# Performance work log

Hardware: AMD Instinct MI355X
Metric: run time of the kernel (lower is better)

## Reference

```python
import jax, jax.numpy as jnp
import numpy as np

CHANNELS = 64
HIDDEN = 1024
LAYERS = 24
NODE_TYPES = 19
BN_EPS = 1e-5

N_NODES = 200000
N_EDGES = 800000
N_RULES = 50000


def setup_inputs() -> dict:
    key = jax.random.key(0)
    ks = jax.random.split(key, 16)
    nodes = jax.random.randint(ks[0], (N_NODES,), 0, NODE_TYPES)
    sources = jax.random.randint(ks[1], (N_EDGES,), 0, N_NODES)
    targets = jax.random.randint(ks[2], (N_EDGES,), 0, N_NODES)
    rules = jax.random.randint(ks[3], (N_RULES,), 0, N_NODES)
    f32 = jnp.float32
    emb = jax.random.normal(ks[4], (NODE_TYPES, CHANNELS), f32)
    # per-layer, per-direction (out/back) Conv params, stacked [LAYERS, 2, ...]
    W = jax.random.normal(ks[5], (LAYERS, 2, CHANNELS, CHANNELS), f32) * 0.125  # ~xavier
    b = jax.random.normal(ks[6], (LAYERS, 2, CHANNELS), f32) * 0.01
    gamma = 1.0 + 0.1 * jax.random.normal(ks[7], (LAYERS, 2, CHANNELS), f32)
    beta = 0.01 * jax.random.normal(ks[8], (LAYERS, 2, CHANNELS), f32)
    rmean = 0.01 * jax.random.normal(ks[9], (LAYERS, 2, CHANNELS), f32)
    rvar = jax.random.uniform(ks[10], (LAYERS, 2, CHANNELS), f32, 0.5, 1.5)
    Wh = jax.random.normal(ks[11], (HIDDEN, CHANNELS), f32) * 0.05
    bh = jax.random.normal(ks[12], (HIDDEN,), f32) * 0.01
    Wo = jax.random.normal(ks[13], (1, HIDDEN), f32) * 0.03
    return {"nodes": nodes, "sources": sources, "targets": targets, "rules": rules,
            "emb": emb, "W": W, "b": b, "gamma": gamma, "beta": beta,
            "rmean": rmean, "rvar": rvar, "Wh": Wh, "bh": bh, "Wo": Wo}


def reference(nodes, sources, targets, rules, emb, W, b, gamma, beta, rmean, rvar, Wh, bh, Wo):
    n = nodes.shape[0]

    def conv(x, src, tgt, Wi, bi, g, be, rm, rv):
        # scatter_mean of gathered source features onto target nodes
        s = jax.ops.segment_sum(x[src], tgt, num_segments=n)            # [n, C]
        cnt = jax.ops.segment_sum(jnp.ones(src.shape, x.dtype), tgt, num_segments=n)
        m = s / jnp.maximum(cnt, 1.0)[:, None]
        # eval-mode BatchNorm1d (running stats) fused as affine
        xn = (m - rm) * (g * jax.lax.rsqrt(rv + BN_EPS)) + be
        return jax.nn.relu(xn @ Wi.T + bi)

    def layer(x, p):
        Wl, bl, gl, bel, rml, rvl = p
        out = conv(x, sources, targets, Wl[0], bl[0], gl[0], bel[0], rml[0], rvl[0])
        back = conv(x, targets, sources, Wl[1], bl[1], gl[1], bel[1], rml[1], rvl[1])
        return x + out + back, None

    x = emb[nodes]                                                      # [n, C]
    x, _ = jax.lax.scan(layer, x, (W, b, gamma, beta, rmean, rvar))
    h = jax.nn.relu(x[rules] @ Wh.T + bh)                               # [R, HIDDEN]
    return (h @ Wo.T)[:, 0]                                             # [R]
```

## Files before the change

kernel.cpp:

```cpp
#include <hip/hip_runtime.h>

#define N_NODES 200000
#define N_EDGES 800000
#define N_RULES 50000
#define NLAYERS 24
#define SCAN_NB 196
#define RP_STRIDE 200064

typedef short bf16x8 __attribute__((ext_vector_type(8)));
typedef float floatx4 __attribute__((ext_vector_type(4)));

__device__ __forceinline__ unsigned short f2bf(float f) {
  unsigned int b = __float_as_uint(f);
  b += 0x7FFFu + ((b >> 16) & 1u);
  return (unsigned short)(b >> 16);
}
__device__ __forceinline__ float bf2f(unsigned short u) {
  return __uint_as_float(((unsigned int)u) << 16);
}


__global__ void k_hist(const int* __restrict__ src, const int* __restrict__ tgt,
                       int* __restrict__ deg_out, int* __restrict__ deg_back) {
  int e = blockIdx.x * 256 + threadIdx.x;
  atomicAdd(&deg_out[tgt[e]], 1);
  atomicAdd(&deg_back[src[e]], 1);
}

__global__ void k_scanA(const int* __restrict__ deg, int* __restrict__ part) {
  int y = blockIdx.y;
  const int* d = deg + y * N_NODES;
  __shared__ int sh[256];
  int t = threadIdx.x;
  int base = blockIdx.x * 1024 + t * 4;
  int s = 0;
  #pragma unroll
  for (int k = 0; k < 4; ++k) { int i = base + k; if (i < N_NODES) s += d[i]; }
  sh[t] = s; __syncthreads();
  for (int off = 128; off > 0; off >>= 1) { if (t < off) sh[t] += sh[t + off]; __syncthreads(); }
  if (t == 0) part[y * SCAN_NB + blockIdx.x] = sh[0];
}

__global__ void k_scanB(int* __restrict__ part, int* __restrict__ rp) {
  int y = blockIdx.y;
  __shared__ int buf[256];
  int t = threadIdx.x;
  int v = (t < SCAN_NB) ? part[y * SCAN_NB + t] : 0;
  buf[t] = v; __syncthreads();
  for (int off = 1; off < 256; off <<= 1) {
    int x = (t >= off) ? buf[t - off] : 0;
    __syncthreads();
    buf[t] += x;
    __syncthreads();
  }
  if (t < SCAN_NB) part[y * SCAN_NB + t] = buf[t] - v;
  if (t == 0) rp[y * RP_STRIDE + N_NODES] = N_EDGES;
}

__global__ void k_scanC(const int* __restrict__ deg, const int* __restrict__ part,
                        int* __restrict__ rp) {
  int y = blockIdx.y;
  const int* d = deg + y * N_NODES;
  int* r = rp + y * RP_STRIDE;
  __shared__ int buf[256];
  int t = threadIdx.x;
  int base = blockIdx.x * 1024 + t * 4;
  int dv[4]; int s = 0;
  #pragma unroll
  for (int k = 0; k < 4; ++k) { int i = base + k; dv[k] = (i < N_NODES) ? d[i] : 0; s += dv[k]; }
  buf[t] = s; __syncthreads();
  int sv = s;
  for (int off = 1; off < 256; off <<= 1) {
    int x = (t >= off) ? buf[t - off] : 0;
    __syncthreads();
    buf[t] += x;
    __syncthreads();
  }
  int e = part[y * SCAN_NB + blockIdx.x] + buf[t] - sv;
  #pragma unroll
  for (int k = 0; k < 4; ++k) { int i = base + k; if (i < N_NODES) r[i] = e; e += dv[k]; }
}

__global__ void k_fill(const int* __restrict__ src, const int* __restrict__ tgt,
                       const int* __restrict__ rp_out, const int* __restrict__ rp_back,
                       int* __restrict__ cur_out, int* __restrict__ cur_back,
                       int* __restrict__ ci_out, int* __restrict__ ci_back) {
  int e = blockIdx.x * 256 + threadIdx.x;
  int s = src[e], t = tgt[e];
  int p = rp_out[t] + atomicAdd(&cur_out[t], 1);
  ci_out[p] = s;
  int q = rp_back[s] + atomicAdd(&cur_back[s], 1);
  ci_back[q] = t;
}

__global__ void k_prep(const float* __restrict__ W, const float* __restrict__ b,
                       const float* __restrict__ gamma, const float* __restrict__ beta,
                       const float* __restrict__ rmean, const float* __restrict__ rvar,
                       unsigned short* __restrict__ WpF, float* __restrict__ bp) {
  int d = blockIdx.x, l = blockIdx.y, lane = threadIdx.x;
  int ld = l * 2 + d;
  __shared__ float s_s[64], t_s[64];
  float s = gamma[ld * 64 + lane] * rsqrtf(rvar[ld * 64 + lane] + 1e-5f);
  s_s[lane] = s;
  t_s[lane] = beta[ld * 64 + lane] - rmean[ld * 64 + lane] * s;
  __syncthreads();
  float bias = b[ld * 64 + lane];
  for (int j = 0; j < 64; ++j) bias += W[(ld * 64 + lane) * 64 + j] * t_s[j];
  bp[ld * 64 + lane] = bias;
  #pragma unroll
  for (int f = 0; f < 8; ++f) {
    int ct = f >> 1, kh = f & 1;
    int row = ct * 16 + (lane & 15);
    #pragma unroll
    for (int jj = 0; jj < 8; ++jj) {
      int k = kh * 32 + (lane >> 4) * 8 + jj;
      float val = W[(ld * 64 + row) * 64 + k] * s_s[k];
      WpF[(ld * 8 + f) * 512 + lane * 8 + jj] = f2bf(val);
    }
  }
}

__global__ void k_prep2(const float* __restrict__ Wh,
                        unsigned short* __restrict__ WhFhi,
                        unsigned short* __restrict__ WhFlo) {
  int jt = blockIdx.x, lane = threadIdx.x;
  #pragma unroll
  for (int kh = 0; kh < 2; ++kh) {
    #pragma unroll
    for (int jj = 0; jj < 8; ++jj) {
      int j = jt * 16 + (lane & 15);
      int k = kh * 32 + (lane >> 4) * 8 + jj;
      float wv = Wh[j * 64 + k];
      unsigned short hi = f2bf(wv);
      WhFhi[(jt * 2 + kh) * 512 + lane * 8 + jj] = hi;
      WhFlo[(jt * 2 + kh) * 512 + lane * 8 + jj] = f2bf(wv - bf2f(hi));
    }
  }
}

__global__ void k_embed(const int* __restrict__ nodes, const float* __restrict__ emb,
                        float* __restrict__ x, unsigned short* __restrict__ xbf) {
  int gid = blockIdx.x * 256 + threadIdx.x;
  int i = gid >> 6, c = gid & 63;
  float v = emb[nodes[i] * 64 + c];
  x[gid] = v;
  xbf[gid] = f2bf(v);
}

__global__ __launch_bounds__(256) void k_layer(
    float* __restrict__ x,
    const unsigned short* __restrict__ xbf_in,
    unsigned short* __restrict__ xbf_out,
    const int* __restrict__ rp0, const int* __restrict__ ci0,
    const int* __restrict__ rp1, const int* __restrict__ ci1,
    const unsigned short* __restrict__ WfL, const float* __restrict__ bpL) {
  __shared__ __align__(16) unsigned short m_s[4][16 * 72];
  __shared__ __align__(16) float y_s[4][16 * 68];
  __shared__ float bp_s[128];
  __shared__ int rp_s[4][18];
  int tid = threadIdx.x, lane = tid & 63, w = tid >> 6;
  if (tid < 128) bp_s[tid] = bpL[tid];
  __syncthreads();
  int base = (blockIdx.x * 4 + w) * 16;
  int n15 = lane & 15, q = lane >> 4;

  for (int d = 0; d < 2; ++d) {
    const int* rp = d ? rp1 : rp0;
    const int* ci = d ? ci1 : ci0;
    if (lane < 17) rp_s[w][lane] = rp[base + lane];
    int rs = __builtin_amdgcn_readfirstlane(rp_s[w][0]);
    int re = __builtin_amdgcn_readfirstlane(rp_s[w][16]);
    int cur = 0;
    int cstart = rs;
    int cend = __builtin_amdgcn_readfirstlane(rp_s[w][1]);
    float acc = 0.f;
    int cv = (rs + lane < re) ? ci[rs + lane] : 0;
    for (int cb = rs; cb < re; cb += 64) {
      int ce = (cb + 64 < re) ? cb + 64 : re;
      int cv_next = (cb + 64 + lane < re) ? ci[cb + 64 + lane] : 0;
      for (int j0 = cb; j0 < ce; j0 += 16) {
        float v[16];
        #pragma unroll
        for (int u = 0; u < 16; ++u) {
          int sn = __builtin_amdgcn_readlane(cv, j0 + u - cb);
          v[u] = bf2f(xbf_in[sn * 64 + lane]);
        }
        #pragma unroll
        for (int u = 0; u < 16; ++u) {
          int j = j0 + u;
          if (j < ce) {
            while (j >= cend) {
              int deg = cend - cstart;
              float invc = deg > 0 ? 1.f / (float)deg : 0.f;
              m_s[w][cur * 72 + lane] = f2bf(acc * invc);
              acc = 0.f; cur++;
              cstart = cend;
              cend = __builtin_amdgcn_readfirstlane(rp_s[w][cur + 1]);
            }
            acc += v[u];
          }
        }
      }
      cv = cv_next;
    }
    #pragma unroll 1
    while (cur < 16) {
      int deg = cend - cstart;
      float invc = deg > 0 ? 1.f / (float)deg : 0.f;
      m_s[w][cur * 72 + lane] = f2bf(acc * invc);
      acc = 0.f; cstart = cend; cur++;
      if (cur < 16) cend = __builtin_amdgcn_readfirstlane(rp_s[w][cur + 1]);
    }

    const unsigned short* wf = WfL + d * 4096;
    bf16x8 b0 = *(const bf16x8*)&m_s[w][n15 * 72 + 0 + q * 8];
    bf16x8 b1 = *(const bf16x8*)&m_s[w][n15 * 72 + 32 + q * 8];
    #pragma unroll
    for (int ct = 0; ct < 4; ++ct) {
      floatx4 a4 = {0.f, 0.f, 0.f, 0.f};
      bf16x8 a0 = *(const bf16x8*)(wf + (ct * 2 + 0) * 512 + lane * 8);
      bf16x8 a1 = *(const bf16x8*)(wf + (ct * 2 + 1) * 512 + lane * 8);
      a4 = __builtin_amdgcn_mfma_f32_16x16x32_bf16(a0, b0, a4, 0, 0, 0);
      a4 = __builtin_amdgcn_mfma_f32_16x16x32_bf16(a1, b1, a4, 0, 0, 0);
      floatx4 yv;
      #pragma unroll
      for (int i = 0; i < 4; ++i)
        yv[i] = fmaxf(a4[i] + bp_s[d * 64 + ct * 16 + q * 4 + i], 0.f);
      float* yp = &y_s[w][n15 * 68 + ct * 16 + q * 4];
      if (d == 0) {
        *(floatx4*)yp = yv;
      } else {
        floatx4 o = *(const floatx4*)yp;
        o += yv;
        *(floatx4*)yp = o;
      }
    }
  }

  #pragma unroll
  for (int r = 0; r < 16; ++r) {
    int gi = (base + r) * 64 + lane;
    float xv = x[gi] + y_s[w][r * 68 + lane];
    x[gi] = xv;
    xbf_out[gi] = f2bf(xv);
  }
}

__global__ __launch_bounds__(256) void k_final(
    const float* __restrict__ x, const int* __restrict__ rules,
    const unsigned short* __restrict__ WhFhi, const unsigned short* __restrict__ WhFlo,
    const float* __restrict__ bh, const float* __restrict__ Wo,
    float* __restrict__ out) {
  __shared__ __align__(16) float bh_s[1024], wo_s[1024];
  int tid = threadIdx.x, lane = tid & 63, w = tid >> 6;
  ((floatx4*)bh_s)[tid] = ((const floatx4*)bh)[tid];
  ((floatx4*)wo_s)[tid] = ((const floatx4*)Wo)[tid];
  __syncthreads();
  int n15 = lane & 15, q = lane >> 4;
  int rbase = (blockIdx.x * 4 + w) * 16;
  int ru = rbase + n15;
  int nd = rules[ru < N_RULES ? ru : N_RULES - 1];
  const float* xr = x + nd * 64;
  floatx4 xa = *(const floatx4*)&xr[q * 8];
  floatx4 xb = *(const floatx4*)&xr[q * 8 + 4];
  floatx4 xc = *(const floatx4*)&xr[32 + q * 8];
  floatx4 xd = *(const floatx4*)&xr[32 + q * 8 + 4];
  bf16x8 b0h, b0l, b1h, b1l;
  #pragma unroll
  for (int i = 0; i < 4; ++i) {
    unsigned short h;
    h = f2bf(xa[i]); b0h[i]     = (short)h; b0l[i]     = (short)f2bf(xa[i] - bf2f(h));
    h = f2bf(xb[i]); b0h[4 + i] = (short)h; b0l[4 + i] = (short)f2bf(xb[i] - bf2f(h));
    h = f2bf(xc[i]); b1h[i]     = (short)h; b1l[i]     = (short)f2bf(xc[i] - bf2f(h));
    h = f2bf(xd[i]); b1h[4 + i] = (short)h; b1l[4 + i] = (short)f2bf(xd[i] - bf2f(h));
  }
  float acc = 0.f;
  #pragma unroll 4
  for (int jt = 0; jt < 64; ++jt) {
    const unsigned short* fh = WhFhi + (jt * 2) * 512 + lane * 8;
    const unsigned short* fl = WhFlo + (jt * 2) * 512 + lane * 8;
    bf16x8 a0h = *(const bf16x8*)fh;
    bf16x8 a1h = *(const bf16x8*)(fh + 512);
    bf16x8 a0l = *(const bf16x8*)fl;
    bf16x8 a1l = *(const bf16x8*)(fl + 512);
    floatx4 d4 = {0.f, 0.f, 0.f, 0.f};
    d4 = __builtin_amdgcn_mfma_f32_16x16x32_bf16(a0h, b0h, d4, 0, 0, 0);
    d4 = __builtin_amdgcn_mfma_f32_16x16x32_bf16(a1h, b1h, d4, 0, 0, 0);
    d4 = __builtin_amdgcn_mfma_f32_16x16x32_bf16(a0h, b0l, d4, 0, 0, 0);
    d4 = __builtin_amdgcn_mfma_f32_16x16x32_bf16(a1h, b1l, d4, 0, 0, 0);
    d4 = __builtin_amdgcn_mfma_f32_16x16x32_bf16(a0l, b0h, d4, 0, 0, 0);
    d4 = __builtin_amdgcn_mfma_f32_16x16x32_bf16(a1l, b1h, d4, 0, 0, 0);
    floatx4 bh4 = *(const floatx4*)&bh_s[jt * 16 + q * 4];
    floatx4 wo4 = *(const floatx4*)&wo_s[jt * 16 + q * 4];
    #pragma unroll
    for (int i = 0; i < 4; ++i)
      acc += fmaxf(d4[i] + bh4[i], 0.f) * wo4[i];
  }
  acc += __shfl_down(acc, 32);
  acc += __shfl_down(acc, 16);
  if (lane < 16 && rbase + lane < N_RULES) out[rbase + lane] = acc;
}

extern "C" void kernel_launch(void* const* d_in, const int* in_sizes, int n_in,
                              void* d_out, int out_size, void* d_ws, size_t ws_size,
                              hipStream_t stream) {
  const int* nodes = (const int*)d_in[0];
  const int* sources = (const int*)d_in[1];
  const int* targets = (const int*)d_in[2];
  const int* rules = (const int*)d_in[3];
  const float* emb = (const float*)d_in[4];
  const float* W = (const float*)d_in[5];
  const float* b = (const float*)d_in[6];
  const float* gamma = (const float*)d_in[7];
  const float* beta = (const float*)d_in[8];
  const float* rmean = (const float*)d_in[9];
  const float* rvar = (const float*)d_in[10];
  const float* Wh = (const float*)d_in[11];
  const float* bh = (const float*)d_in[12];
  const float* Wo = (const float*)d_in[13];
  float* out = (float*)d_out;

  if (ws_size < 114270000u) return;

  char* ws = (char*)d_ws;
  float* x = (float*)(ws + 0);
  unsigned short* xbf_a = (unsigned short*)(ws + 51200000);
  unsigned short* xbf_b = (unsigned short*)(ws + 76800000);
  int* deg_out = (int*)(ws + 102400000);
  int* deg_back = deg_out + N_NODES;
  int* cur_out = (int*)(ws + 104000000);
  int* cur_back = (int*)(ws + 104800000);
  int* rp_out = (int*)(ws + 105600000);
  int* rp_back = rp_out + RP_STRIDE;
  int* ci_out = (int*)(ws + 107200512);
  int* ci_back = (int*)(ws + 110400512);
  int* part = (int*)(ws + 113600512);
  unsigned short* WpF = (unsigned short*)(ws + 113602096);
  float* bp = (float*)(ws + 113995312);
  unsigned short* WhFhi = (unsigned short*)(ws + 114007600);
  unsigned short* WhFlo = (unsigned short*)(ws + 114138672);

  hipMemsetAsync(deg_out, 0, 3200000u, stream);

  k_hist<<<3125, 256, 0, stream>>>(sources, targets, deg_out, deg_back);
  k_scanA<<<dim3(SCAN_NB, 2), 256, 0, stream>>>(deg_out, part);
  k_scanB<<<dim3(1, 2), 256, 0, stream>>>(part, rp_out);
  k_scanC<<<dim3(SCAN_NB, 2), 256, 0, stream>>>(deg_out, part, rp_out);
  k_fill<<<3125, 256, 0, stream>>>(sources, targets, rp_out, rp_back,
                                   cur_out, cur_back, ci_out, ci_back);
  k_prep<<<dim3(2, NLAYERS), 64, 0, stream>>>(W, b, gamma, beta, rmean, rvar, WpF, bp);
  k_prep2<<<64, 64, 0, stream>>>(Wh, WhFhi, WhFlo);
  k_embed<<<50000, 256, 0, stream>>>(nodes, emb, x, xbf_a);

  const unsigned short* bi = xbf_a;
  unsigned short* bo = xbf_b;
  for (int l = 0; l < NLAYERS; ++l) {
    k_layer<<<3125, 256, 0, stream>>>(x, bi, bo, rp_out, ci_out, rp_back, ci_back,
                                      WpF + (size_t)l * 8192, bp + (size_t)l * 128);
    const unsigned short* t = bi; bi = bo; bo = (unsigned short*)t;
  }
  k_final<<<782, 256, 0, stream>>>(x, rules, WhFhi, WhFlo, bh, Wo, out);
}
```

Baseline: 1.848 ms.

## Double-buffer neighbor gathers and keep layer outputs in registers

The gather loop in the per-layer kernel now processes neighbors in 16-edge batches with two register buffers, issuing the next batch's bf16 loads before accumulating the current one so memory latency overlaps the segment-mean work. The LDS staging for row pointers, bias and the MFMA output tile is removed: row pointers are read with readlane from a register, bias comes straight from global memory, and MFMA results accumulate in registers and are written back as vectorized float4 and short4 stores. This also drops a block-wide barrier. The cost is higher register pressure, and the ci loads can now read past the edge list (indices are masked), which relies on padding.

Measured after the change: 1.991 ms. +7.7%, slower.

```diff
diff --git a/kernel.cpp b/kernel.cpp
--- a/kernel.cpp
+++ b/kernel.cpp
@@ -9,6 +9,7 @@
 
 typedef short bf16x8 __attribute__((ext_vector_type(8)));
 typedef float floatx4 __attribute__((ext_vector_type(4)));
+typedef short shortx4 __attribute__((ext_vector_type(4)));
 
 __device__ __forceinline__ unsigned short f2bf(float f) {
   unsigned int b = __float_as_uint(f);
@@ -155,94 +156,112 @@
     const int* __restrict__ rp1, const int* __restrict__ ci1,
     const unsigned short* __restrict__ WfL, const float* __restrict__ bpL) {
   __shared__ __align__(16) unsigned short m_s[4][16 * 72];
-  __shared__ __align__(16) float y_s[4][16 * 68];
-  __shared__ float bp_s[128];
-  __shared__ int rp_s[4][18];
   int tid = threadIdx.x, lane = tid & 63, w = tid >> 6;
-  if (tid < 128) bp_s[tid] = bpL[tid];
-  __syncthreads();
   int base = (blockIdx.x * 4 + w) * 16;
   int n15 = lane & 15, q = lane >> 4;
-
+  float y[16];
+
+  #pragma unroll
   for (int d = 0; d < 2; ++d) {
     const int* rp = d ? rp1 : rp0;
     const int* ci = d ? ci1 : ci0;
-    if (lane < 17) rp_s[w][lane] = rp[base + lane];
-    int rs = __builtin_amdgcn_readfirstlane(rp_s[w][0]);
-    int re = __builtin_amdgcn_readfirstlane(rp_s[w][16]);
-    int cur = 0;
-    int cstart = rs;
-    int cend = __builtin_amdgcn_readfirstlane(rp_s[w][1]);
+    int rpv = rp[base + (lane < 17 ? lane : 16)];
+    int rs = __builtin_amdgcn_readlane(rpv, 0);
+    int re = __builtin_amdgcn_readlane(rpv, 16);
+    int cur = 0, cstart = rs;
+    int cend = __builtin_amdgcn_readlane(rpv, 1);
     float acc = 0.f;
-    int cv = (rs + lane < re) ? ci[rs + lane] : 0;
-    for (int cb = rs; cb < re; cb += 64) {
-      int ce = (cb + 64 < re) ? cb + 64 : re;
-      int cv_next = (cb + 64 + lane < re) ? ci[cb + 64 + lane] : 0;
-      for (int j0 = cb; j0 < ce; j0 += 16) {
-        float v[16];
-        #pragma unroll
-        for (int u = 0; u < 16; ++u) {
-          int sn = __builtin_amdgcn_readlane(cv, j0 + u - cb);
-          v[u] = bf2f(xbf_in[sn * 64 + lane]);
+    int cv_cur = ci[rs + lane];
+    int cv_nxt = ci[rs + 64 + lane];
+    int nb = (re - rs + 15) >> 4;
+    unsigned short v0[16], v1[16];
+
+#define ISSUE(buf, b)                                                      \
+    {                                                                      \
+      int bb_ = ((b) & 3) << 4;                                            \
+      _Pragma("unroll")                                                    \
+      for (int u = 0; u < 16; ++u) {                                       \
+        int sn = __builtin_amdgcn_readlane(cv_cur, bb_ + u) & 0x3FFFF;     \
+        buf[u] = xbf_in[sn * 64 + lane];                                   \
+      }                                                                    \
+    }
+#define CONSUME(buf, b)                                                    \
+    {                                                                      \
+      int jb_ = rs + (b) * 16;                                             \
+      _Pragma("unroll")                                                    \
+      for (int u = 0; u < 16; ++u) {                                       \
+        int j = jb_ + u;                                                   \
+        if (j < re) {                                                      \
+          while (j >= cend) {                                              \
+            int deg = cend - cstart;                                       \
+            float invc = deg > 0 ? 1.f / (float)deg : 0.f;                 \
+            m_s[w][cur * 72 + lane] = f2bf(acc * invc);                    \
+            acc = 0.f; cur++; cstart = cend;                               \
+            cend = __builtin_amdgcn_readlane(rpv, cur + 1);                \
+          }                                                                \
+          acc += bf2f(buf[u]);                                             \
+        }                                                                  \
+      }                                                                    \
+    }
+
+    if (nb > 0) ISSUE(v0, 0);
+    int i = 0;
+    for (; i + 2 <= nb; i += 2) {
+      ISSUE(v1, i + 1);
+      CONSUME(v0, i);
+      if (i + 2 < nb) {
+        if (((i + 2) & 3) == 0) {
+          cv_cur = cv_nxt;
+          cv_nxt = ci[rs + (i + 2) * 16 + 64 + lane];
         }
-        #pragma unroll
-        for (int u = 0; u < 16; ++u) {
-          int j = j0 + u;
-          if (j < ce) {
-            while (j >= cend) {
-              int deg = cend - cstart;
-              float invc = deg > 0 ? 1.f / (float)deg : 0.f;
-              m_s[w][cur * 72 + lane] = f2bf(acc * invc);
-              acc = 0.f; cur++;
-              cstart = cend;
-              cend = __builtin_amdgcn_readfirstlane(rp_s[w][cur + 1]);
-            }
-            acc += v[u];
-          }
-        }
+        ISSUE(v0, i + 2);
       }
-      cv = cv_next;
-    }
+      CONSUME(v1, i + 1);
+    }
+    if (i < nb) CONSUME(v0, i);
+#undef ISSUE
+#undef CONSUME
+
     #pragma unroll 1
     while (cur < 16) {
       int deg = cend - cstart;
       float invc = deg > 0 ? 1.f / (float)deg : 0.f;
       m_s[w][cur * 72 + lane] = f2bf(acc * invc);
       acc = 0.f; cstart = cend; cur++;
-      if (cur < 16) cend = __builtin_amdgcn_readfirstlane(rp_s[w][cur + 1]);
+      if (cur < 16) cend = __builtin_amdgcn_readlane(rpv, cur + 1);
     }
 
     const unsigned short* wf = WfL + d * 4096;
-    bf16x8 b0 = *(const bf16x8*)&m_s[w][n15 * 72 + 0 + q * 8];
+    bf16x8 b0 = *(const bf16x8*)&m_s[w][n15 * 72 + q * 8];
     bf16x8 b1 = *(const bf16x8*)&m_s[w][n15 * 72 + 32 + q * 8];
     #pragma unroll
     for (int ct = 0; ct < 4; ++ct) {
-      floatx4 a4 = {0.f, 0.f, 0.f, 0.f};
+      floatx4 d4 = {0.f, 0.f, 0.f, 0.f};
       bf16x8 a0 = *(const bf16x8*)(wf + (ct * 2 + 0) * 512 + lane * 8);
       bf16x8 a1 = *(const bf16x8*)(wf + (ct * 2 + 1) * 512 + lane * 8);
-      a4 = __builtin_amdgcn_mfma_f32_16x16x32_bf16(a0, b0, a4, 0, 0, 0);
-      a4 = __builtin_amdgcn_mfma_f32_16x16x32_bf16(a1, b1, a4, 0, 0, 0);
-      floatx4 yv;
+      d4 = __builtin_amdgcn_mfma_f32_16x16x32_bf16(a0, b0, d4, 0, 0, 0);
+      d4 = __builtin_amdgcn_mfma_f32_16x16x32_bf16(a1, b1, d4, 0, 0, 0);
+      floatx4 bp4 = *(const floatx4*)(bpL + d * 64 + ct * 16 + q * 4);
       #pragma unroll
-      for (int i = 0; i < 4; ++i)
-        yv[i] = fmaxf(a4[i] + bp_s[d * 64 + ct * 16 + q * 4 + i], 0.f);
-      float* yp = &y_s[w][n15 * 68 + ct * 16 + q * 4];
-      if (d == 0) {
-        *(floatx4*)yp = yv;
-      } else {
-        floatx4 o = *(const floatx4*)yp;
-        o += yv;
-        *(floatx4*)yp = o;
+      for (int i2 = 0; i2 < 4; ++i2) {
+        float yv = fmaxf(d4[i2] + bp4[i2], 0.f);
+        if (d == 0) y[ct * 4 + i2] = yv; else y[ct * 4 + i2] += yv;
       }
     }
   }
 
-  #pragma unroll
-  for (int r = 0; r < 16; ++r) {
-    int gi = (base + r) * 64 + lane;
-    float xv = x[gi] + y_s[w][r * 68 + lane];
-    x[gi] = xv;
-    xbf_out[gi] = f2bf(xv);
+  int nrow = base + n15;
+  #pragma unroll
+  for (int ct = 0; ct < 4; ++ct) {
+    float* xp = &x[nrow * 64 + ct * 16 + q * 4];
+    floatx4 xo = *(const floatx4*)xp;
+    #pragma unroll
+    for (int i2 = 0; i2 < 4; ++i2) xo[i2] += y[ct * 4 + i2];
+    *(floatx4*)xp = xo;
+    shortx4 hb;
+    #pragma unroll
+    for (int i2 = 0; i2 < 4; ++i2) hb[i2] = (short)f2bf(xo[i2]);
+    *(shortx4*)&xbf_out[nrow * 64 + ct * 16 + q * 4] = hb;
   }
 }
 
```
